# Performance work log

Hardware: AMD Instinct MI355X
Metric: run time of the kernel (lower is better)

Reference implementation:

```python
import jax, jax.numpy as jnp
import numpy as np

K = 4
G = 64
IN_DIM = 256
OUT_DIM = 256
BATCH = 512
T0, T1 = -1.0, 1.0


def setup_inputs() -> dict:
    key = jax.random.key(0)
    kx, kw = jax.random.split(key)
    x = jax.random.uniform(kx, (BATCH, IN_DIM), jnp.float32, T0, T1)
    # xavier_normal_ on [G+K, in, out]: std = sqrt(2 / (fan_in + fan_out)) with fan over last two dims
    std = (2.0 / (IN_DIM + OUT_DIM)) ** 0.5
    w = jax.random.normal(kw, (G + K, IN_DIM, OUT_DIM), jnp.float32) * std
    # knot vector: k-1 repeats of t0, linspace(t0,t1,G+1), k-1 repeats of t1
    t = jnp.concatenate([
        jnp.full((K - 1,), T0, jnp.float32),
        jnp.linspace(T0, T1, G + 1, dtype=jnp.float32),
        jnp.full((K - 1,), T1, jnp.float32),
    ])
    return {"x": x, "w": w, "t": t, "k": K}


def _basis(x, t, k):
    """Cox-de Boor: the k nonzero order-k B-spline basis values at each x.
    Returns (idx, N): idx [..., k] basis indices i-k+1..i, N [..., k] values."""
    n_t = t.shape[0]
    # interval i with t[i] <= x < t[i+1], clipped to the valid span
    i = jnp.clip(jnp.searchsorted(t, x, side='right') - 1, k - 1, n_t - k - 1)
    N = jnp.ones(x.shape + (1,), x.dtype)
    for p in range(1, k):  # static small loop (k=4)
        jj = jnp.arange(1, p + 1)
        left = x[..., None] - t[i[..., None] + 1 - jj]   # [..., p]
        right = t[i[..., None] + jj] - x[..., None]      # [..., p]
        saved = jnp.zeros_like(x)
        vals = []
        for r in range(p):
            d = right[..., r] + left[..., p - 1 - r]      # t[i+r+1] - t[i+r+1-p]
            temp = N[..., r] / d
            vals.append(saved + right[..., r] * temp)
            saved = left[..., p - 1 - r] * temp
        vals.append(saved)
        N = jnp.stack(vals, -1)
    idx = i[..., None] - (k - 1) + jnp.arange(k)
    return idx, N


def reference(x, w, t, k):
    in_dim = x.shape[1]
    n_rows = w.shape[0]
    idx, y1 = _basis(x, t, k)                             # [B,in,k], [B,in,k]
    # last row of w (index -1 == n_rows-1) weights the SiLU residual term
    idx_full = jnp.concatenate(
        [idx, jnp.full(idx.shape[:-1] + (1,), n_rows - 1, idx.dtype)], -1)  # [B,in,k+1]
    silu = x * jax.nn.sigmoid(x)
    y2 = jnp.concatenate([y1, silu[..., None]], -1)       # [B,in,k+1]
    # gather local spline coefficients: w2[b,c,j,o] = w[idx_full[b,c,j], c, o]
    w2 = w[idx_full, jnp.arange(in_dim)[None, :, None], :]  # [B,in,k+1,out]
    return jnp.einsum('bcjo,bcj->bo', w2, y2)             # [B,out]
```

## Files before the change

kernel.cpp:

```cpp
#include <hip/hip_runtime.h>
#include <math.h>
#include <stdint.h>

#define IN_DIM  256
#define OUT_DIM 256
#define NROWS   68
#define NT      71
#define BATCH   512
#define W_ELEMS (NROWS * IN_DIM * OUT_DIM)
#define NCG     16
#define PART_FLOATS (NCG * BATCH * OUT_DIM)

__device__ __forceinline__ uint32_t bf16_rne(float f) {
  uint32_t u = __builtin_bit_cast(uint32_t, f);
  return (u + 0x7fffu + ((u >> 16) & 1u)) >> 16;
}

__global__ __launch_bounds__(256) void cvt_kernel(const float* __restrict__ w,
                                                  uint32_t* __restrict__ wb) {
  const int base = (blockIdx.x * 256 + threadIdx.x) * 8;
  const float4 a = *(const float4*)(w + base);
  const float4 b = *(const float4*)(w + base + 4);
  uint4 o;
  o.x = bf16_rne(a.x) | (bf16_rne(a.y) << 16);
  o.y = bf16_rne(a.z) | (bf16_rne(a.w) << 16);
  o.z = bf16_rne(b.x) | (bf16_rne(b.y) << 16);
  o.w = bf16_rne(b.z) | (bf16_rne(b.w) << 16);
  *(uint4*)(wb + base / 2) = o;
}

__device__ __forceinline__ void fma8(const uint4 q, const float y, float* acc) {
  acc[0] += y * __builtin_bit_cast(float, q.x << 16);
  acc[1] += y * __builtin_bit_cast(float, q.x & 0xffff0000u);
  acc[2] += y * __builtin_bit_cast(float, q.y << 16);
  acc[3] += y * __builtin_bit_cast(float, q.y & 0xffff0000u);
  acc[4] += y * __builtin_bit_cast(float, q.z << 16);
  acc[5] += y * __builtin_bit_cast(float, q.z & 0xffff0000u);
  acc[6] += y * __builtin_bit_cast(float, q.w << 16);
  acc[7] += y * __builtin_bit_cast(float, q.w & 0xffff0000u);
}

__global__ __launch_bounds__(256) void kan_gather_kernel(
    const float* __restrict__ x, const uint4* __restrict__ wp,
    const float* __restrict__ t, float* __restrict__ part) {
  __shared__ float  lt[NT];
  __shared__ float4 nA[16][32];
  __shared__ float  sA[16][32];
  __shared__ int    bA[16][32];
  __shared__ uint4  lbuf[NROWS * 32];

  const int tid = threadIdx.x;
  const unsigned bid = blockIdx.x;
  const int cg     = bid & 15;
  const int bgroup = bid >> 4;

  if (tid < NT) lt[tid] = t[tid];
  __syncthreads();

  for (int p = tid; p < 512; p += 256) {
    const int cl = p >> 5;
    const int bb = p & 31;
    const float xv = x[(size_t)(bgroup * 32 + bb) * IN_DIM + cg * 16 + cl];
    int i = 3 + (int)floorf((xv + 1.0f) * 32.0f);
    i = i < 3 ? 3 : (i > 66 ? 66 : i);
    while (i > 3 && xv < lt[i]) --i;
    while (i < 66 && xv >= lt[i + 1]) ++i;

    float N0 = 1.f, N1 = 0.f, N2 = 0.f, N3 = 0.f;
    {
      const float l1 = xv - lt[i];
      const float r1 = lt[i + 1] - xv;
      const float tp = N0 / (r1 + l1);
      N1 = l1 * tp; N0 = r1 * tp;
    }
    {
      const float l1 = xv - lt[i];
      const float l2 = xv - lt[i - 1];
      const float r1 = lt[i + 1] - xv;
      const float r2 = lt[i + 2] - xv;
      float saved = 0.f;
      const float tp0 = N0 / (r1 + l2);
      const float n0 = saved + r1 * tp0; saved = l2 * tp0;
      const float tp1 = N1 / (r2 + l1);
      const float n1 = saved + r2 * tp1; saved = l1 * tp1;
      N0 = n0; N1 = n1; N2 = saved;
    }
    {
      const float l1 = xv - lt[i];
      const float l2 = xv - lt[i - 1];
      const float l3 = xv - lt[i - 2];
      const float r1 = lt[i + 1] - xv;
      const float r2 = lt[i + 2] - xv;
      const float r3 = lt[i + 3] - xv;
      float saved = 0.f;
      const float tp0 = N0 / (r1 + l3);
      const float n0 = saved + r1 * tp0; saved = l3 * tp0;
      const float tp1 = N1 / (r2 + l2);
      const float n1 = saved + r2 * tp1; saved = l2 * tp1;
      const float tp2 = N2 / (r3 + l1);
      const float n2 = saved + r3 * tp2; saved = l1 * tp2;
      N0 = n0; N1 = n1; N2 = n2; N3 = saved;
    }
    nA[cl][bb] = make_float4(N0, N1, N2, N3);
    sA[cl][bb] = xv / (1.0f + expf(-xv));
    bA[cl][bb] = i - 3;
  }
  __syncthreads();

  const int wv   = tid >> 6;
  const int lane = tid & 63;
  const int half = lane >> 5;
  const int ol   = lane & 31;

  float acc[4][8];
  #pragma unroll
  for (int bp = 0; bp < 4; ++bp) {
    #pragma unroll
    for (int j = 0; j < 8; ++j) acc[bp][j] = 0.f;
  }

  for (int ch = 0; ch < 16; ++ch) {
    {
      const uint32_t cb = (uint32_t)(cg * 16 + ch) * 32;
      for (int i = wv; i < 34; i += 4) {
        const int Xu = i * 64 + lane;
        const int r  = Xu >> 5;
        const int off = Xu & 31;
        const uint4* src = wp + ((uint32_t)r << 13) + cb + off;
        __builtin_amdgcn_global_load_lds((const uint32_t*)src,
                                         (uint32_t*)&lbuf[i * 64], 16, 0, 0);
      }
    }
    __syncthreads();

    const uint4 q4 = lbuf[67 * 32 + ol];
    #pragma unroll
    for (int bp = 0; bp < 4; ++bp) {
      const int bb = wv * 8 + bp * 2 + half;
      const float4 yv = nA[ch][bb];
      const float  ys = sA[ch][bb];
      const int    rb = bA[ch][bb] * 32 + ol;
      const uint4 q0 = lbuf[rb];
      const uint4 q1 = lbuf[rb + 32];
      const uint4 q2 = lbuf[rb + 64];
      const uint4 q3 = lbuf[rb + 96];
      fma8(q0, yv.x, acc[bp]);
      fma8(q1, yv.y, acc[bp]);
      fma8(q2, yv.z, acc[bp]);
      fma8(q3, yv.w, acc[bp]);
      fma8(q4, ys,   acc[bp]);
    }
    __syncthreads();
  }

  {
    float* dst = part + ((size_t)cg * BATCH + bgroup * 32) * OUT_DIM;
    #pragma unroll
    for (int bp = 0; bp < 4; ++bp) {
      const int bb = wv * 8 + bp * 2 + half;
      float* d = dst + (size_t)bb * OUT_DIM + ol * 8;
      *(float4*)d       = make_float4(acc[bp][0], acc[bp][1], acc[bp][2], acc[bp][3]);
      *(float4*)(d + 4) = make_float4(acc[bp][4], acc[bp][5], acc[bp][6], acc[bp][7]);
    }
  }
}

__global__ __launch_bounds__(256) void reduce_kernel(const float* __restrict__ part,
                                                     float* __restrict__ out) {
  const int q = blockIdx.x * 256 + threadIdx.x;
  const int S = BATCH * OUT_DIM / 4;
  const float4* p = (const float4*)part;
  float4 s = p[q];
  #pragma unroll
  for (int k = 1; k < NCG; ++k) {
    const float4 a = p[q + k * S];
    s.x += a.x; s.y += a.y; s.z += a.z; s.w += a.w;
  }
  ((float4*)out)[q] = s;
}

extern "C" void kernel_launch(void* const* d_in, const int* in_sizes, int n_in,
                              void* d_out, int out_size, void* d_ws, size_t ws_size,
                              hipStream_t stream) {
  const float* x = (const float*)d_in[0];
  const float* w = (const float*)d_in[1];
  const float* t = (const float*)d_in[2];
  float* out  = (float*)d_out;
  float* part = (float*)d_ws;
  uint32_t* wb = (uint32_t*)d_ws + PART_FLOATS;
  cvt_kernel<<<W_ELEMS / (256 * 8), 256, 0, stream>>>(w, wb);
  kan_gather_kernel<<<256, 256, 0, stream>>>(x, (const uint4*)wb, t, part);
  reduce_kernel<<<BATCH * OUT_DIM / 4 / 256, 256, 0, stream>>>(part, out);
}
```

Measured before the change: 100.5 us.

## Gather spline weights directly from global memory and double channel groups

Drops the per-channel bulk copy of all 68 weight rows into LDS. Each thread now loads only the four basis rows it needs plus the SiLU row straight from global memory. The channel dimension is split into 32 groups instead of 16, which doubles the grid to 512 blocks and halves the per-block channel loop. In exchange, the partial-sum buffer and the reduction work double, and the global loads are data-dependent and less coalesced, relying on L2 caching of the bf16 weights.

Result: faster. 94.07 us (-6.4%).

```diff
diff --git a/kernel.cpp b/kernel.cpp
--- a/kernel.cpp
+++ b/kernel.cpp
@@ -8,7 +8,7 @@
 #define NT      71
 #define BATCH   512
 #define W_ELEMS (NROWS * IN_DIM * OUT_DIM)
-#define NCG     16
+#define NCG     32
 #define PART_FLOATS (NCG * BATCH * OUT_DIM)
 
 __device__ __forceinline__ uint32_t bf16_rne(float f) {
@@ -44,23 +44,22 @@
     const float* __restrict__ x, const uint4* __restrict__ wp,
     const float* __restrict__ t, float* __restrict__ part) {
   __shared__ float  lt[NT];
-  __shared__ float4 nA[16][32];
-  __shared__ float  sA[16][32];
-  __shared__ int    bA[16][32];
-  __shared__ uint4  lbuf[NROWS * 32];
+  __shared__ float4 nA[8][32];
+  __shared__ float  sA[8][32];
+  __shared__ int    bA[8][32];
 
   const int tid = threadIdx.x;
   const unsigned bid = blockIdx.x;
-  const int cg     = bid & 15;
-  const int bgroup = bid >> 4;
+  const int cg     = bid & 31;
+  const int bgroup = bid >> 5;
 
   if (tid < NT) lt[tid] = t[tid];
   __syncthreads();
 
-  for (int p = tid; p < 512; p += 256) {
-    const int cl = p >> 5;
-    const int bb = p & 31;
-    const float xv = x[(size_t)(bgroup * 32 + bb) * IN_DIM + cg * 16 + cl];
+  {
+    const int cl = tid & 7;
+    const int bb = tid >> 3;
+    const float xv = x[(size_t)(bgroup * 32 + bb) * IN_DIM + cg * 8 + cl];
     int i = 3 + (int)floorf((xv + 1.0f) * 32.0f);
     i = i < 3 ? 3 : (i > 66 ? 66 : i);
     while (i > 3 && xv < lt[i]) --i;
@@ -114,53 +113,47 @@
 
   float acc[4][8];
   #pragma unroll
-  for (int bp = 0; bp < 4; ++bp) {
+  for (int p = 0; p < 4; ++p) {
     #pragma unroll
-    for (int j = 0; j < 8; ++j) acc[bp][j] = 0.f;
+    for (int j = 0; j < 8; ++j) acc[p][j] = 0.f;
   }
 
-  for (int ch = 0; ch < 16; ++ch) {
-    {
-      const uint32_t cb = (uint32_t)(cg * 16 + ch) * 32;
-      for (int i = wv; i < 34; i += 4) {
-        const int Xu = i * 64 + lane;
-        const int r  = Xu >> 5;
-        const int off = Xu & 31;
-        const uint4* src = wp + ((uint32_t)r << 13) + cb + off;
-        __builtin_amdgcn_global_load_lds((const uint32_t*)src,
-                                         (uint32_t*)&lbuf[i * 64], 16, 0, 0);
-      }
+  for (int ch = 0; ch < 8; ++ch) {
+    const uint32_t cbase = (uint32_t)((cg * 8 + ch) * 32 + ol);
+    const uint4 q4 = wp[cbase + 67u * 8192u];
+
+    uint4 q[4][4];
+    #pragma unroll
+    for (int p = 0; p < 4; ++p) {
+      const int bb = wv * 8 + p * 2 + half;
+      const uint32_t rb = cbase + ((uint32_t)bA[ch][bb] << 13);
+      q[p][0] = wp[rb];
+      q[p][1] = wp[rb +  8192u];
+      q[p][2] = wp[rb + 16384u];
+      q[p][3] = wp[rb + 24576u];
     }
-    __syncthreads();
-
-    const uint4 q4 = lbuf[67 * 32 + ol];
     #pragma unroll
-    for (int bp = 0; bp < 4; ++bp) {
-      const int bb = wv * 8 + bp * 2 + half;
+    for (int p = 0; p < 4; ++p) {
+      const int bb = wv * 8 + p * 2 + half;
       const float4 yv = nA[ch][bb];
       const float  ys = sA[ch][bb];
-      const int    rb = bA[ch][bb] * 32 + ol;
-      const uint4 q0 = lbuf[rb];
-      const uint4 q1 = lbuf[rb + 32];
-      const uint4 q2 = lbuf[rb + 64];
-      const uint4 q3 = lbuf[rb + 96];
-      fma8(q0, yv.x, acc[bp]);
-      fma8(q1, yv.y, acc[bp]);
-      fma8(q2, yv.z, acc[bp]);
-      fma8(q3, yv.w, acc[bp]);
-      fma8(q4, ys,   acc[bp]);
+      fma8(q[p][0], yv.x, acc[p]);
+      fma8(q[p][1], yv.y, acc[p]);
+      fma8(q[p][2], yv.z, acc[p]);
+      fma8(q[p][3], yv.w, acc[p]);
+      fma8(q4,      ys,   acc[p]);
     }
     __syncthreads();
   }
 
   {
-    float* dst = part + ((size_t)cg * BATCH + bgroup * 32) * OUT_DIM;
+    float* dst0 = part + ((size_t)cg * BATCH + bgroup * 32) * OUT_DIM;
     #pragma unroll
-    for (int bp = 0; bp < 4; ++bp) {
-      const int bb = wv * 8 + bp * 2 + half;
-      float* d = dst + (size_t)bb * OUT_DIM + ol * 8;
-      *(float4*)d       = make_float4(acc[bp][0], acc[bp][1], acc[bp][2], acc[bp][3]);
-      *(float4*)(d + 4) = make_float4(acc[bp][4], acc[bp][5], acc[bp][6], acc[bp][7]);
+    for (int p = 0; p < 4; ++p) {
+      const int bb = wv * 8 + p * 2 + half;
+      float* d = dst0 + (size_t)bb * OUT_DIM + ol * 8;
+      *(float4*)d       = make_float4(acc[p][0], acc[p][1], acc[p][2], acc[p][3]);
+      *(float4*)(d + 4) = make_float4(acc[p][4], acc[p][5], acc[p][6], acc[p][7]);
     }
   }
 }
@@ -189,6 +182,6 @@
   float* part = (float*)d_ws;
   uint32_t* wb = (uint32_t*)d_ws + PART_FLOATS;
   cvt_kernel<<<W_ELEMS / (256 * 8), 256, 0, stream>>>(w, wb);
-  kan_gather_kernel<<<256, 256, 0, stream>>>(x, (const uint4*)wb, t, part);
+  kan_gather_kernel<<<512, 256, 0, stream>>>(x, (const uint4*)wb, t, part);
   reduce_kernel<<<BATCH * OUT_DIM / 4 / 256, 256, 0, stream>>>(part, out);
 }
```
